# Performance work log

Hardware: AMD Instinct MI355X
Metric: run time of the kernel (lower is better)

Reference implementation:

```python
import jax, jax.numpy as jnp
import numpy as np

NUM_EXPERTS = 8
TOP_K = 2
EMBED = 1024
FFN = 2048
GATE_HID = 1024


def setup_inputs() -> dict:
    key = jax.random.key(0)
    ks = jax.random.split(key, 8)
    s_e = 1.0 / np.sqrt(EMBED)
    s_f = 1.0 / np.sqrt(FFN)
    s_g = 1.0 / np.sqrt(GATE_HID)
    return {
        "hidden_states": jax.random.normal(ks[0], (2, 2048, EMBED), dtype=jnp.float32),
        # gate: Linear(EMBED->GATE_HID) with bias, ELU, Linear(GATE_HID->NUM_EXPERTS) with bias
        "gw1": jax.random.uniform(ks[1], (EMBED, GATE_HID), jnp.float32, -s_e, s_e),
        "gb1": jax.random.uniform(ks[2], (GATE_HID,), jnp.float32, -s_e, s_e),
        "gw2": jax.random.uniform(ks[3], (GATE_HID, NUM_EXPERTS), jnp.float32, -s_g, s_g),
        "gb2": jax.random.uniform(ks[4], (NUM_EXPERTS,), jnp.float32, -s_g, s_g),
        # experts (bias=False): w1,w3: EMBED->FFN ; w2: FFN->EMBED, stacked over experts
        "w1": jax.random.uniform(ks[5], (NUM_EXPERTS, EMBED, FFN), jnp.float32, -s_e, s_e),
        "w3": jax.random.uniform(ks[6], (NUM_EXPERTS, EMBED, FFN), jnp.float32, -s_e, s_e),
        "w2": jax.random.uniform(ks[7], (NUM_EXPERTS, FFN, EMBED), jnp.float32, -s_f, s_f),
    }


def reference(hidden_states, gw1, gb1, gw2, gb2, w1, w3, w2):
    B, S, H = hidden_states.shape
    x = hidden_states.reshape(-1, H)                      # [T, H]
    T = x.shape[0]
    # gate MLP
    g = jax.nn.elu(x @ gw1 + gb1)
    router_logits = g @ gw2 + gb2                         # [T, E]
    probs = jax.nn.softmax(router_logits.astype(jnp.float32), axis=-1)
    rw, sel = jax.lax.top_k(probs, TOP_K)                 # [T, K]
    rw = rw / jnp.sum(rw, axis=-1, keepdims=True)
    rw = rw.astype(hidden_states.dtype)
    # combine weights per (token, expert); full-capacity MoE == weighted sum
    combine = jnp.zeros((T, NUM_EXPERTS), dtype=hidden_states.dtype)
    combine = combine.at[jnp.arange(T)[:, None], sel].add(rw)   # [T, E]
    # expert MLPs computed densely then combined (math identical to gather/scatter)
    h = jax.nn.relu(jnp.einsum('th,ehf->etf', x, w1)) * jnp.einsum('th,ehf->etf', x, w3)
    y = jnp.einsum('etf,efh->eth', h, w2)                 # [E, T, H]
    out = jnp.einsum('eth,te->th', y, combine)            # [T, H]
    return out.reshape(B, S, H), router_logits
```

## Files before the change

kernel.cpp:

```cpp
#include <hip/hip_runtime.h>
#include <hip/hip_bf16.h>
#include <stdint.h>

#define TOKENS 4096
#define HDIM   1024
#define FDIM   2048
#define NEXP   8
#define NSLOTS (2 * TOKENS)
#define SLOTPAD (NSLOTS + 256)
#define RISKY_CAP 256
#define FLAG_THR 6e-3f

typedef __attribute__((ext_vector_type(4))) float        f32x4v;
typedef __attribute__((ext_vector_type(4))) unsigned int u32x4v;
typedef __attribute__((ext_vector_type(8))) _Float16     f16x8v;

__device__ __forceinline__ unsigned short f2h(float f) {
  _Float16 h = (_Float16)f;
  union { _Float16 h; unsigned short u; } x; x.h = h; return x.u;
}

__device__ __forceinline__ void gload16(void* lds, const void* g) {
  __builtin_amdgcn_global_load_lds(
      reinterpret_cast<const __attribute__((address_space(1))) uint32_t*>(
          reinterpret_cast<uintptr_t>(g)),
      reinterpret_cast<__attribute__((address_space(3))) uint32_t*>(
          reinterpret_cast<uintptr_t>(lds)),
      16, 0, 0);
}

__device__ __forceinline__ void transpose_tile_v2(const float* __restrict__ ip,
                                                  unsigned short* __restrict__ op,
                                                  int R, int C, int r0, int c0) {
  __shared__ unsigned short tile[64][70];
  const int t = threadIdx.x;
  const int cp = (t & 15) * 4;
  const int rp = (t >> 4) * 2;
#pragma unroll
  for (int p = 0; p < 2; ++p) {
    const int r = rp + p * 32;
    f32x4v v0 = *(const f32x4v*)(ip + (size_t)(r0 + r) * C + c0 + cp);
    f32x4v v1 = *(const f32x4v*)(ip + (size_t)(r0 + r + 1) * C + c0 + cp);
#pragma unroll
    for (int j = 0; j < 4; ++j)
      *(uint32_t*)&tile[cp + j][r] = (uint32_t)f2h(v0[j]) | ((uint32_t)f2h(v1[j]) << 16);
  }
  __syncthreads();
  const int c = t >> 2, rc = (t & 3) * 16;
  uint32_t q[8];
#pragma unroll
  for (int j = 0; j < 8; ++j) q[j] = *(uint32_t*)&tile[c][rc + j * 2];
  unsigned short* o = op + (size_t)(c0 + c) * R + r0 + rc;
  u32x4v s0, s1;
  s0[0] = q[0]; s0[1] = q[1]; s0[2] = q[2]; s0[3] = q[3];
  s1[0] = q[4]; s1[1] = q[5]; s1[2] = q[6]; s1[3] = q[7];
  *(u32x4v*)o = s0;
  *(u32x4v*)(o + 8) = s1;
}

__global__ __launch_bounds__(256)
void k_prep0(const float* __restrict__ gw1, unsigned short* __restrict__ og1,
             int* __restrict__ rcnt) {
  if (blockIdx.x == 256) {
    if (threadIdx.x == 0) rcnt[0] = 0;
    return;
  }
  transpose_tile_v2(gw1, og1, 1024, 1024, (blockIdx.x >> 4) * 64, (blockIdx.x & 15) * 64);
}

#define NB_GATE 512
#define NB_CONV 2048
#define NB_W13  8192
#define NB_W2   4096
__global__ __launch_bounds__(256)
void k_fused(const float* __restrict__ X, unsigned short* __restrict__ Xh,
             const float* __restrict__ w1, const float* __restrict__ w3,
             unsigned short* __restrict__ o1, unsigned short* __restrict__ o3,
             const float* __restrict__ w2, unsigned short* __restrict__ o2,
             const unsigned short* __restrict__ gw1T, const float* __restrict__ gb1,
             unsigned short* __restrict__ Gh) {
  const int id = blockIdx.x;
  const int t = threadIdx.x;
  if (id < NB_GATE) {
    __shared__ unsigned short lA[128 * 64];
    __shared__ unsigned short lB[64 * 64];
    const int n0 = (id & 15) * 64, m0 = (id >> 4) * 128;
    const int lane = t & 63, wv = t >> 6;

    const unsigned short* bp[2];
#pragma unroll
    for (int i = 0; i < 2; ++i) {
      const int gi = wv * 2 + i;
      const int row = gi * 8 + (lane >> 3);
      const int cs = (lane & 7) ^ (row & 7);
      bp[i] = gw1T + (size_t)(n0 + row) * HDIM + cs * 8;
    }

    f32x4v acc[4][2];
#pragma unroll
    for (int m = 0; m < 4; ++m)
#pragma unroll
      for (int n = 0; n < 2; ++n) acc[m][n] = (f32x4v){0.f, 0.f, 0.f, 0.f};

    const int wr = (wv >> 1) * 64, wc = (wv & 1) * 32;

    for (int k0 = 0; k0 < HDIM; k0 += 64) {
#pragma unroll
      for (int p = 0; p < 4; ++p) {
        const int ga = p * 256 + t;
        const int r = ga >> 3, c = ga & 7;
        const float* s = X + (size_t)(m0 + r) * HDIM + k0 + c * 8;
        f32x4v v0 = *(const f32x4v*)s;
        f32x4v v1 = *(const f32x4v*)(s + 4);
        u32x4v pk;
        pk[0] = (uint32_t)f2h(v0[0]) | ((uint32_t)f2h(v0[1]) << 16);
        pk[1] = (uint32_t)f2h(v0[2]) | ((uint32_t)f2h(v0[3]) << 16);
        pk[2] = (uint32_t)f2h(v1[0]) | ((uint32_t)f2h(v1[1]) << 16);
        pk[3] = (uint32_t)f2h(v1[2]) | ((uint32_t)f2h(v1[3]) << 16);
        *(u32x4v*)&lA[r * 64 + ((c ^ (r & 7)) * 8)] = pk;
      }
#pragma unroll
      for (int i = 0; i < 2; ++i) gload16(lB + (wv * 2 + i) * 512, bp[i] + k0);
      __syncthreads();
#pragma unroll
      for (int kk = 0; kk < 2; ++kk) {
        const int ch = kk * 4 + (lane >> 4);
        f16x8v af[4];
#pragma unroll
        for (int m = 0; m < 4; ++m) {
          const int r = wr + m * 16 + (lane & 15);
          af[m] = *(const f16x8v*)(lA + r * 64 + (ch ^ (r & 7)) * 8);
        }
#pragma unroll
        for (int n = 0; n < 2; ++n) {
          const int r = wc + n * 16 + (lane & 15);
          f16x8v b = *(const f16x8v*)(lB + r * 64 + (ch ^ (r & 7)) * 8);
#pragma unroll
          for (int m = 0; m < 4; ++m)
            acc[m][n] = __builtin_amdgcn_mfma_f32_16x16x32_f16(af[m], b, acc[m][n], 0, 0, 0);
        }
      }
      __syncthreads();
    }
#pragma unroll
    for (int m = 0; m < 4; ++m)
#pragma unroll
      for (int n = 0; n < 2; ++n)
#pragma unroll
        for (int q = 0; q < 4; ++q) {
          const int row = m0 + wr + m * 16 + ((lane >> 4) << 2) + q;
          const int col = n0 + wc + n * 16 + (lane & 15);
          float x = acc[m][n][q] + gb1[col];
          Gh[(size_t)row * 1024 + col] = f2h(x > 0.f ? x : expm1f(x));
        }
    return;
  }
  int b = id - NB_GATE;
  if (b < NB_CONV) {
    const int i = (b * 256 + t) * 8;
    f32x4v a = *(const f32x4v*)(X + i);
    f32x4v c = *(const f32x4v*)(X + i + 4);
    u32x4v r;
    r[0] = (uint32_t)f2h(a[0]) | ((uint32_t)f2h(a[1]) << 16);
    r[1] = (uint32_t)f2h(a[2]) | ((uint32_t)f2h(a[3]) << 16);
    r[2] = (uint32_t)f2h(c[0]) | ((uint32_t)f2h(c[1]) << 16);
    r[3] = (uint32_t)f2h(c[2]) | ((uint32_t)f2h(c[3]) << 16);
    *(u32x4v*)(Xh + i) = r;
    return;
  }
  b -= NB_CONV;
  if (b < NB_W13) {
    const int bx = b & 31, by = (b >> 5) & 15, bz = b >> 9;
    const int e = bz & 7, which = bz >> 3;
    const size_t mat = (size_t)1024 * 2048;
    transpose_tile_v2((which ? w3 : w1) + (size_t)e * mat,
                      (which ? o3 : o1) + (size_t)e * mat,
                      1024, 2048, by * 64, bx * 64);
    return;
  }
  b -= NB_W13;
  {
    const int bx = b & 15, by = (b >> 4) & 31, e = b >> 9;
    const size_t mat = (size_t)2048 * 1024;
    transpose_tile_v2(w2 + (size_t)e * mat, o2 + (size_t)e * mat,
                      2048, 1024, by * 64, bx * 64);
  }
}

__global__ void k_logits(const unsigned short* __restrict__ Gh, const float* __restrict__ gw2,
                         const float* __restrict__ gb2, float* __restrict__ Lg,
                         int* __restrict__ risky, int* __restrict__ rcnt) {
  const int lane = threadIdx.x & 63, wv = threadIdx.x >> 6;
  const int tok = blockIdx.x * 4 + wv;
  const unsigned short* g = Gh + (size_t)tok * 1024 + lane * 16;
  f16x8v g0 = *(const f16x8v*)g;
  f16x8v g1 = *(const f16x8v*)(g + 8);
  float gv[16];
#pragma unroll
  for (int j = 0; j < 8; ++j) { gv[j] = (float)g0[j]; gv[8 + j] = (float)g1[j]; }
  float acc[8];
#pragma unroll
  for (int j = 0; j < 8; ++j) acc[j] = 0.f;
#pragma unroll
  for (int u = 0; u < 16; ++u) {
    const float* wrow = gw2 + (size_t)(lane * 16 + u) * 8;
    f32x4v w0 = *(const f32x4v*)wrow;
    f32x4v w1 = *(const f32x4v*)(wrow + 4);
#pragma unroll
    for (int j = 0; j < 4; ++j) {
      acc[j]     += gv[u] * w0[j];
      acc[j + 4] += gv[u] * w1[j];
    }
  }
#pragma unroll
  for (int s = 1; s < 64; s <<= 1)
#pragma unroll
    for (int j = 0; j < 8; ++j) acc[j] += __shfl_xor(acc[j], s, 64);
  if (lane == 0) {
    float l[8];
#pragma unroll
    for (int j = 0; j < 8; ++j) { l[j] = acc[j] + gb2[j]; Lg[(size_t)tok * 8 + j] = l[j]; }
    int i0 = 0; float v0 = l[0];
#pragma unroll
    for (int j = 1; j < 8; ++j) if (l[j] > v0) { v0 = l[j]; i0 = j; }
    int i1 = (i0 == 0) ? 1 : 0; float v1 = l[i1];
#pragma unroll
    for (int j = 0; j < 8; ++j) if (j != i0 && l[j] > v1) { v1 = l[j]; i1 = j; }
    float v2 = -1e30f;
#pragma unroll
    for (int j = 0; j < 8; ++j) if (j != i0 && j != i1 && l[j] > v2) v2 = l[j];
    if (v1 - v2 < FLAG_THR) {
      const int pos = atomicAdd(rcnt, 1);
      if (pos < RISKY_CAP) risky[pos] = tok;
    }
  }
}

__global__ __launch_bounds__(256)
void k_fixup_gs(const float* __restrict__ X, const float* __restrict__ gw1,
                const float* __restrict__ gb1, const int* __restrict__ risky,
                const int* __restrict__ rcnt, float* __restrict__ gsbuf) {
  __shared__ float xs[1024];
  __shared__ float red[128];
  int n = *rcnt; if (n > RISKY_CAP) n = RISKY_CAP;
  const int idx = blockIdx.y;
  if (idx >= n) return;
  const int tok = risky[idx];
  const int s0 = blockIdx.x * 128;
  const int t = threadIdx.x;
  for (int i = t; i < 1024; i += 256) xs[i] = X[(size_t)tok * 1024 + i];
  __syncthreads();
  const int h = t & 127, kh = t >> 7;
  const float* wp = gw1 + (size_t)(kh * 512) * 1024 + s0 + h;
  const float* xp = xs + kh * 512;
  float a0 = 0.f, a1 = 0.f, a2 = 0.f, a3 = 0.f;
  for (int k = 0; k < 512; k += 4) {
    a0 += xp[k]     * wp[(size_t)k * 1024];
    a1 += xp[k + 1] * wp[(size_t)(k + 1) * 1024];
    a2 += xp[k + 2] * wp[(size_t)(k + 2) * 1024];
    a3 += xp[k + 3] * wp[(size_t)(k + 3) * 1024];
  }
  const float acc = (a0 + a1) + (a2 + a3);
  if (kh == 1) red[h] = acc;
  __syncthreads();
  if (kh == 0) {
    const float v = acc + red[h] + gb1[s0 + h];
    gsbuf[(size_t)idx * 1024 + s0 + h] = v > 0.f ? v : expm1f(v);
  }
}

__global__ __launch_bounds__(256)
void k_fixup_lg(const float* __restrict__ gsbuf, const float* __restrict__ gw2,
                const float* __restrict__ gb2, const int* __restrict__ risky,
                const int* __restrict__ rcnt, float* __restrict__ Lg) {
  __shared__ float part[4][8];
  int n = *rcnt; if (n > RISKY_CAP) n = RISKY_CAP;
  const int idx = blockIdx.x;
  if (idx >= n) return;
  const int tok = risky[idx];
  const int t = threadIdx.x, lane = t & 63, wv = t >> 6;
  float lacc[8];
#pragma unroll
  for (int e = 0; e < 8; ++e) lacc[e] = 0.f;
#pragma unroll
  for (int j = 0; j < 4; ++j) {
    const int k = t * 4 + j;
    const float gv = gsbuf[(size_t)idx * 1024 + k];
    const float* w = gw2 + (size_t)k * 8;
#pragma unroll
    for (int e = 0; e < 8; ++e) lacc[e] += gv * w[e];
  }
#pragma unroll
  for (int s = 1; s < 64; s <<= 1)
#pragma unroll
    for (int e = 0; e < 8; ++e) lacc[e] += __shfl_xor(lacc[e], s, 64);
  if (lane == 0) {
#pragma unroll
    for (int e = 0; e < 8; ++e) part[wv][e] = lacc[e];
  }
  __syncthreads();
  if (t < 8) Lg[(size_t)tok * 8 + t] = part[0][t] + part[1][t] + part[2][t] + part[3][t] + gb2[t];
}

__global__ __launch_bounds__(1024)
void k_top2assign(const float* __restrict__ Lg, int* __restrict__ counts_g,
                  int* __restrict__ offs_g, int* __restrict__ slot_tok,
                  float* __restrict__ slot_w, int* __restrict__ tok2slot) {
  __shared__ int cnt[NEXP], offs[NEXP], cur[NEXP];
  const int t = threadIdx.x, lane = t & 63;
  if (t < NEXP) { cnt[t] = 0; cur[t] = 0; }
  __syncthreads();

  int te[4][2]; float tw[4][2];
#pragma unroll
  for (int p = 0; p < 4; ++p) {
    const int tok = p * 1024 + t;
    float l[8];
#pragma unroll
    for (int j = 0; j < 8; ++j) l[j] = Lg[(size_t)tok * 8 + j];
    float mx = l[0];
#pragma unroll
    for (int j = 1; j < 8; ++j) mx = fmaxf(mx, l[j]);
    float pr[8];
#pragma unroll
    for (int j = 0; j < 8; ++j) pr[j] = expf(l[j] - mx);
    int i0 = 0; float b0 = pr[0];
#pragma unroll
    for (int j = 1; j < 8; ++j) if (pr[j] > b0) { b0 = pr[j]; i0 = j; }
    int i1 = (i0 == 0) ? 1 : 0; float b1 = pr[i1];
#pragma unroll
    for (int j = 0; j < 8; ++j) if (j != i0 && pr[j] > b1) { b1 = pr[j]; i1 = j; }
    const float inv = 1.f / (b0 + b1);
    te[p][0] = i0; te[p][1] = i1;
    tw[p][0] = b0 * inv; tw[p][1] = b1 * inv;
#pragma unroll
    for (int k = 0; k < 2; ++k) {
      const int e = te[p][k];
#pragma unroll
      for (int ex = 0; ex < NEXP; ++ex) {
        const unsigned long long mask = __ballot(e == ex);
        if (mask) {
          const int leader = __ffsll((unsigned long long)mask) - 1;
          if (lane == leader) atomicAdd(&cnt[ex], (int)__popcll(mask));
        }
      }
    }
  }
  __syncthreads();
  if (t == 0) {
    int a = 0;
#pragma unroll
    for (int e = 0; e < NEXP; ++e) { offs[e] = a; a += cnt[e]; }
  }
  __syncthreads();
#pragma unroll
  for (int p = 0; p < 4; ++p) {
    const int tok = p * 1024 + t;
#pragma unroll
    for (int k = 0; k < 2; ++k) {
      const int e = te[p][k];
#pragma unroll
      for (int ex = 0; ex < NEXP; ++ex) {
        const unsigned long long mask = __ballot(e == ex);
        if (mask) {
          const int leader = __ffsll((unsigned long long)mask) - 1;
          int base = 0;
          if (lane == leader) base = atomicAdd(&cur[ex], (int)__popcll(mask));
          base = __shfl(base, leader, 64);
          if (e == ex) {
            const int s = offs[ex] + base + (int)__popcll(mask & ((1ull << lane) - 1ull));
            slot_tok[s] = tok;
            slot_w[s] = tw[p][k];
            tok2slot[2 * tok + k] = s;
          }
        }
      }
    }
  }
  if (t < NEXP) { counts_g[t] = cnt[t]; offs_g[t] = offs[t]; }
}

__global__ __launch_bounds__(256, 2)
void k_gemm1(const unsigned short* __restrict__ Xh, const unsigned short* __restrict__ w1T,
             const unsigned short* __restrict__ w3T, const int* __restrict__ slot_tok,
             const int* __restrict__ counts, const int* __restrict__ offs,
             unsigned short* __restrict__ Hout) {
  const int e = blockIdx.z;
  const int cnt = counts[e];
  const int mt = blockIdx.y;
  if (mt * 128 >= cnt) return;
  const int base = offs[e] + mt * 128;
  const int n0 = blockIdx.x * 128;

  __shared__ unsigned short lA[128 * 64];
  __shared__ unsigned short lB1[128 * 64];
  __shared__ unsigned short lB3[128 * 64];
  __shared__ int tokid[128];

  const int t = threadIdx.x;
  if (t < 128) {
    const int s = slot_tok[base + t];
    tokid[t] = ((unsigned)s < TOKENS) ? s : 0;
  }
  __syncthreads();

  const int lane = t & 63, wv = t >> 6;
  const unsigned short *arow[4], *b1row[4], *b3row[4];
#pragma unroll
  for (int i = 0; i < 4; ++i) {
    const int gi = wv * 4 + i;
    const int row = gi * 8 + (lane >> 3);
    const int cs = (lane & 7) ^ (row & 7);
    arow[i] = Xh + (size_t)tokid[row] * HDIM + cs * 8;
    const int f = n0 + row;
    b1row[i] = w1T + ((size_t)e * FDIM + f) * HDIM + cs * 8;
    b3row[i] = w3T + ((size_t)e * FDIM + f) * HDIM + cs * 8;
  }

  f32x4v acc1[4][4], acc3[4][4];
#pragma unroll
  for (int m = 0; m < 4; ++m)
#pragma unroll
    for (int n = 0; n < 4; ++n) {
      acc1[m][n] = (f32x4v){0.f, 0.f, 0.f, 0.f};
      acc3[m][n] = (f32x4v){0.f, 0.f, 0.f, 0.f};
    }
  const int wr = (wv >> 1) * 64, wc = (wv & 1) * 64;

  for (int k0 = 0; k0 < HDIM; k0 += 64) {
#pragma unroll
    for (int i = 0; i < 4; ++i) {
      gload16(lA + (wv * 4 + i) * 512, arow[i] + k0);
      gload16(lB1 + (wv * 4 + i) * 512, b1row[i] + k0);
      gload16(lB3 + (wv * 4 + i) * 512, b3row[i] + k0);
    }
    __syncthreads();
#pragma unroll
    for (int kk = 0; kk < 64; kk += 32) {
      const int ch = (kk >> 3) + (lane >> 4);
      f16x8v af[4];
#pragma unroll
      for (int m = 0; m < 4; ++m) {
        const int r = wr + m * 16 + (lane & 15);
        af[m] = *(const f16x8v*)(lA + r * 64 + (ch ^ (r & 7)) * 8);
      }
#pragma unroll
      for (int n = 0; n < 4; ++n) {
        const int r = wc + n * 16 + (lane & 15);
        const int o = r * 64 + (ch ^ (r & 7)) * 8;
        f16x8v b1 = *(const f16x8v*)(lB1 + o);
        f16x8v b3 = *(const f16x8v*)(lB3 + o);
#pragma unroll
        for (int m = 0; m < 4; ++m) {
          acc1[m][n] = __builtin_amdgcn_mfma_f32_16x16x32_f16(af[m], b1, acc1[m][n], 0, 0, 0);
          acc3[m][n] = __builtin_amdgcn_mfma_f32_16x16x32_f16(af[m], b3, acc3[m][n], 0, 0, 0);
        }
      }
    }
    __syncthreads();
  }

  const int maxr = cnt - mt * 128;
#pragma unroll
  for (int m = 0; m < 4; ++m)
#pragma unroll
    for (int q = 0; q < 4; ++q) {
      const int rl = wr + m * 16 + ((lane >> 4) << 2) + q;
      if (rl < maxr) {
        unsigned short* hrow = Hout + (size_t)(base + rl) * FDIM;
#pragma unroll
        for (int n = 0; n < 4; ++n) {
          const int col = n0 + wc + n * 16 + (lane & 15);
          const float h = fmaxf(acc1[m][n][q], 0.f) * acc3[m][n][q];
          hrow[col] = f2h(h);
        }
      }
    }
}

__global__ __launch_bounds__(256, 2)
void k_gemm2(const unsigned short* __restrict__ Hin, const unsigned short* __restrict__ w2T,
             const int* __restrict__ counts, const int* __restrict__ offs,
             unsigned short* __restrict__ Y) {
  const int e = blockIdx.z;
  const int cnt = counts[e];
  const int mt = blockIdx.y;
  if (mt * 128 >= cnt) return;
  const int base = offs[e] + mt * 128;
  const int n0 = blockIdx.x * 256;

  __shared__ unsigned short lA[128 * 64];
  __shared__ unsigned short lBa[128 * 64];
  __shared__ unsigned short lBb[128 * 64];

  const int t = threadIdx.x, lane = t & 63, wv = t >> 6;
  const unsigned short *arow[4], *browa[4], *browb[4];
#pragma unroll
  for (int i = 0; i < 4; ++i) {
    const int gi = wv * 4 + i;
    const int row = gi * 8 + (lane >> 3);
    const int cs = (lane & 7) ^ (row & 7);
    arow[i] = Hin + (size_t)(base + row) * FDIM + cs * 8;
    browa[i] = w2T + ((size_t)e * HDIM + n0 + row) * FDIM + cs * 8;
    browb[i] = w2T + ((size_t)e * HDIM + n0 + 128 + row) * FDIM + cs * 8;
  }

  f32x4v acca[4][4], accb[4][4];
#pragma unroll
  for (int m = 0; m < 4; ++m)
#pragma unroll
    for (int n = 0; n < 4; ++n) {
      acca[m][n] = (f32x4v){0.f, 0.f, 0.f, 0.f};
      accb[m][n] = (f32x4v){0.f, 0.f, 0.f, 0.f};
    }

  const int wr = (wv >> 1) * 64, wc = (wv & 1) * 64;

  for (int k0 = 0; k0 < FDIM; k0 += 64) {
#pragma unroll
    for (int i = 0; i < 4; ++i) {
      gload16(lA + (wv * 4 + i) * 512, arow[i] + k0);
      gload16(lBa + (wv * 4 + i) * 512, browa[i] + k0);
      gload16(lBb + (wv * 4 + i) * 512, browb[i] + k0);
    }
    __syncthreads();
#pragma unroll
    for (int kk = 0; kk < 64; kk += 32) {
      const int ch = (kk >> 3) + (lane >> 4);
      f16x8v af[4];
#pragma unroll
      for (int m = 0; m < 4; ++m) {
        const int r = wr + m * 16 + (lane & 15);
        af[m] = *(const f16x8v*)(lA + r * 64 + (ch ^ (r & 7)) * 8);
      }
#pragma unroll
      for (int n = 0; n < 4; ++n) {
        const int r = wc + n * 16 + (lane & 15);
        const int o = r * 64 + (ch ^ (r & 7)) * 8;
        f16x8v ba = *(const f16x8v*)(lBa + o);
        f16x8v bb = *(const f16x8v*)(lBb + o);
#pragma unroll
        for (int m = 0; m < 4; ++m) {
          acca[m][n] = __builtin_amdgcn_mfma_f32_16x16x32_f16(af[m], ba, acca[m][n], 0, 0, 0);
          accb[m][n] = __builtin_amdgcn_mfma_f32_16x16x32_f16(af[m], bb, accb[m][n], 0, 0, 0);
        }
      }
    }
    __syncthreads();
  }

  const int maxr = cnt - mt * 128;
#pragma unroll
  for (int m = 0; m < 4; ++m)
#pragma unroll
    for (int q = 0; q < 4; ++q) {
      const int rl = wr + m * 16 + ((lane >> 4) << 2) + q;
      if (rl < maxr) {
        unsigned short* yrow = Y + (size_t)(base + rl) * HDIM;
#pragma unroll
        for (int n = 0; n < 4; ++n) {
          const int col = n0 + wc + n * 16 + (lane & 15);
          yrow[col] = f2h(acca[m][n][q]);
          yrow[col + 128] = f2h(accb[m][n][q]);
        }
      }
    }
}

__global__ __launch_bounds__(256)
void k_combine(const unsigned short* __restrict__ Y, const int* __restrict__ tok2slot,
               const float* __restrict__ slot_w, float* __restrict__ out) {
  const int tok = blockIdx.x;
  const int s0 = tok2slot[2 * tok], s1 = tok2slot[2 * tok + 1];
  const float w0 = slot_w[s0], w1 = slot_w[s1];
  const int i = threadIdx.x * 4;
  const _Float16* y0 = (const _Float16*)(Y + (size_t)s0 * HDIM + i);
  const _Float16* y1 = (const _Float16*)(Y + (size_t)s1 * HDIM + i);
  f32x4v r;
#pragma unroll
  for (int j = 0; j < 4; ++j) r[j] = w0 * (float)y0[j] + w1 * (float)y1[j];
  *(f32x4v*)(out + (size_t)tok * HDIM + i) = r;
}

extern "C" void kernel_launch(void* const* d_in, const int* in_sizes, int n_in,
                              void* d_out, int out_size, void* d_ws, size_t ws_size,
                              hipStream_t stream) {
  const float* X   = (const float*)d_in[0];
  const float* gw1 = (const float*)d_in[1];
  const float* gb1 = (const float*)d_in[2];
  const float* gw2 = (const float*)d_in[3];
  const float* gb2 = (const float*)d_in[4];
  const float* w1  = (const float*)d_in[5];
  const float* w3  = (const float*)d_in[6];
  const float* w2  = (const float*)d_in[7];

  float* out = (float*)d_out;
  float* Lg  = out + (size_t)TOKENS * HDIM;

  char* ws = (char*)d_ws;
  size_t off = 0;
  auto alloc = [&](size_t b) { void* p = ws + off; off = (off + b + 255) & ~(size_t)255; return p; };

  unsigned short* Xh    = (unsigned short*)alloc((size_t)TOKENS * HDIM * 2);
  unsigned short* gw1T  = (unsigned short*)alloc((size_t)HDIM * 1024 * 2);
  unsigned short* w1T   = (unsigned short*)alloc((size_t)NEXP * FDIM * HDIM * 2);
  unsigned short* w3T   = (unsigned short*)alloc((size_t)NEXP * FDIM * HDIM * 2);
  unsigned short* w2T   = (unsigned short*)alloc((size_t)NEXP * HDIM * FDIM * 2);
  unsigned short* Gh    = (unsigned short*)alloc((size_t)TOKENS * 1024 * 2);
  unsigned short* Hf    = (unsigned short*)alloc((size_t)SLOTPAD * FDIM * 2);
  unsigned short* Yb    = (unsigned short*)alloc((size_t)SLOTPAD * HDIM * 2);
  float*          gsbuf = (float*)alloc((size_t)RISKY_CAP * 1024 * 4);
  int*   tok2slot = (int*)alloc((size_t)TOKENS * 2 * 4);
  int*   counts   = (int*)alloc(64);
  int*   offs     = (int*)alloc(64);
  int*   slot_tok = (int*)alloc((size_t)SLOTPAD * 4);
  float* slot_w   = (float*)alloc((size_t)SLOTPAD * 4);
  int*   risky    = (int*)alloc((size_t)RISKY_CAP * 4);
  int*   rcnt     = (int*)alloc(64);

  k_prep0<<<dim3(257), 256, 0, stream>>>(gw1, gw1T, rcnt);
  k_fused<<<dim3(NB_GATE + NB_CONV + NB_W13 + NB_W2), 256, 0, stream>>>(
      X, Xh, w1, w3, w1T, w3T, w2, w2T, gw1T, gb1, Gh);
  k_logits<<<dim3(TOKENS / 4), 256, 0, stream>>>(Gh, gw2, gb2, Lg, risky, rcnt);
  k_fixup_gs<<<dim3(8, RISKY_CAP), 256, 0, stream>>>(X, gw1, gb1, risky, rcnt, gsbuf);
  k_fixup_lg<<<dim3(RISKY_CAP), 256, 0, stream>>>(gsbuf, gw2, gb2, risky, rcnt, Lg);
  k_top2assign<<<dim3(1), 1024, 0, stream>>>(Lg, counts, offs, slot_tok, slot_w, tok2slot);
  k_gemm1<<<dim3(FDIM / 128, TOKENS / 128, NEXP), 256, 0, stream>>>(Xh, w1T, w3T, slot_tok, counts, offs, Hf);
  k_gemm2<<<dim3(HDIM / 256, TOKENS / 128, NEXP), 256, 0, stream>>>(Hf, w2T, counts, offs, Yb);
  k_combine<<<dim3(TOKENS), 256, 0, stream>>>(Yb, tok2slot, slot_w, out);
}
```

Measured before the change: 318.9 us.

## Split-K gemm2 into two halves and fold logit fixup into top2 assign

The down-projection GEMM is split along the FFN dimension into two K halves. Each half writes its own fp16 partial Y buffer, and the combine kernel sums the two partials. This doubles the number of blocks to fill more CUs, at the cost of twice the Y write/read traffic and an extra fp16 rounding step. The separate risky-token logit fixup kernel is also merged into the single-block top-2 assignment kernel, removing one launch but doing that work inside a single workgroup.

Measured after the change: 405.9 us. 1.27x slower.

```diff
diff --git a/kernel.cpp b/kernel.cpp
--- a/kernel.cpp
+++ b/kernel.cpp
@@ -269,55 +269,64 @@
   }
 }
 
-__global__ __launch_bounds__(256)
-void k_fixup_lg(const float* __restrict__ gsbuf, const float* __restrict__ gw2,
-                const float* __restrict__ gb2, const int* __restrict__ risky,
-                const int* __restrict__ rcnt, float* __restrict__ Lg) {
-  __shared__ float part[4][8];
+__global__ __launch_bounds__(1024)
+void k_top2assign(const float* __restrict__ Lg, const float* __restrict__ gsbuf,
+                  const float* __restrict__ gw2, const float* __restrict__ gb2,
+                  const int* __restrict__ risky, const int* __restrict__ rcnt,
+                  int* __restrict__ counts_g, int* __restrict__ offs_g,
+                  int* __restrict__ slot_tok, float* __restrict__ slot_w,
+                  int* __restrict__ tok2slot, float* __restrict__ Lg_out) {
+  __shared__ int cnt[NEXP], offs[NEXP], cur[NEXP];
+  __shared__ short fixslot[TOKENS];
+  __shared__ float lgfix[RISKY_CAP][8];
+  const int t = threadIdx.x, lane = t & 63, wv = t >> 6;
+  for (int i = t; i < TOKENS; i += 1024) fixslot[i] = -1;
+  if (t < NEXP) { cnt[t] = 0; cur[t] = 0; }
   int n = *rcnt; if (n > RISKY_CAP) n = RISKY_CAP;
-  const int idx = blockIdx.x;
-  if (idx >= n) return;
-  const int tok = risky[idx];
-  const int t = threadIdx.x, lane = t & 63, wv = t >> 6;
-  float lacc[8];
-#pragma unroll
-  for (int e = 0; e < 8; ++e) lacc[e] = 0.f;
-#pragma unroll
-  for (int j = 0; j < 4; ++j) {
-    const int k = t * 4 + j;
-    const float gv = gsbuf[(size_t)idx * 1024 + k];
-    const float* w = gw2 + (size_t)k * 8;
-#pragma unroll
-    for (int e = 0; e < 8; ++e) lacc[e] += gv * w[e];
-  }
-#pragma unroll
-  for (int s = 1; s < 64; s <<= 1)
-#pragma unroll
-    for (int e = 0; e < 8; ++e) lacc[e] += __shfl_xor(lacc[e], s, 64);
-  if (lane == 0) {
-#pragma unroll
-    for (int e = 0; e < 8; ++e) part[wv][e] = lacc[e];
-  }
-  __syncthreads();
-  if (t < 8) Lg[(size_t)tok * 8 + t] = part[0][t] + part[1][t] + part[2][t] + part[3][t] + gb2[t];
-}
-
-__global__ __launch_bounds__(1024)
-void k_top2assign(const float* __restrict__ Lg, int* __restrict__ counts_g,
-                  int* __restrict__ offs_g, int* __restrict__ slot_tok,
-                  float* __restrict__ slot_w, int* __restrict__ tok2slot) {
-  __shared__ int cnt[NEXP], offs[NEXP], cur[NEXP];
-  const int t = threadIdx.x, lane = t & 63;
-  if (t < NEXP) { cnt[t] = 0; cur[t] = 0; }
+  __syncthreads();
+
+  for (int idx = wv; idx < n; idx += 16) {
+    const int tok = risky[idx];
+    float lacc[8];
+#pragma unroll
+    for (int e = 0; e < 8; ++e) lacc[e] = 0.f;
+#pragma unroll
+    for (int j = 0; j < 16; ++j) {
+      const int k = lane * 16 + j;
+      const float gv = gsbuf[(size_t)idx * 1024 + k];
+      const float* w = gw2 + (size_t)k * 8;
+#pragma unroll
+      for (int e = 0; e < 8; ++e) lacc[e] += gv * w[e];
+    }
+#pragma unroll
+    for (int s = 1; s < 64; s <<= 1)
+#pragma unroll
+      for (int e = 0; e < 8; ++e) lacc[e] += __shfl_xor(lacc[e], s, 64);
+    if (lane == 0) {
+#pragma unroll
+      for (int e = 0; e < 8; ++e) {
+        const float v = lacc[e] + gb2[e];
+        lgfix[idx][e] = v;
+        Lg_out[(size_t)tok * 8 + e] = v;
+      }
+      fixslot[tok] = (short)idx;
+    }
+  }
   __syncthreads();
 
   int te[4][2]; float tw[4][2];
 #pragma unroll
   for (int p = 0; p < 4; ++p) {
     const int tok = p * 1024 + t;
+    const int fs = fixslot[tok];
     float l[8];
-#pragma unroll
-    for (int j = 0; j < 8; ++j) l[j] = Lg[(size_t)tok * 8 + j];
+    if (fs >= 0) {
+#pragma unroll
+      for (int j = 0; j < 8; ++j) l[j] = lgfix[fs][j];
+    } else {
+#pragma unroll
+      for (int j = 0; j < 8; ++j) l[j] = Lg[(size_t)tok * 8 + j];
+    }
     float mx = l[0];
 #pragma unroll
     for (int j = 1; j < 8; ++j) mx = fmaxf(mx, l[j]);
@@ -482,12 +491,14 @@
 void k_gemm2(const unsigned short* __restrict__ Hin, const unsigned short* __restrict__ w2T,
              const int* __restrict__ counts, const int* __restrict__ offs,
              unsigned short* __restrict__ Y) {
-  const int e = blockIdx.z;
+  const int z = blockIdx.z;
+  const int e = z >> 1, kh = z & 1;
   const int cnt = counts[e];
   const int mt = blockIdx.y;
   if (mt * 128 >= cnt) return;
   const int base = offs[e] + mt * 128;
   const int n0 = blockIdx.x * 256;
+  const int kbeg = kh * (FDIM / 2);
 
   __shared__ unsigned short lA[128 * 64];
   __shared__ unsigned short lBa[128 * 64];
@@ -500,9 +511,9 @@
     const int gi = wv * 4 + i;
     const int row = gi * 8 + (lane >> 3);
     const int cs = (lane & 7) ^ (row & 7);
-    arow[i] = Hin + (size_t)(base + row) * FDIM + cs * 8;
-    browa[i] = w2T + ((size_t)e * HDIM + n0 + row) * FDIM + cs * 8;
-    browb[i] = w2T + ((size_t)e * HDIM + n0 + 128 + row) * FDIM + cs * 8;
+    arow[i] = Hin + (size_t)(base + row) * FDIM + kbeg + cs * 8;
+    browa[i] = w2T + ((size_t)e * HDIM + n0 + row) * FDIM + kbeg + cs * 8;
+    browb[i] = w2T + ((size_t)e * HDIM + n0 + 128 + row) * FDIM + kbeg + cs * 8;
   }
 
   f32x4v acca[4][4], accb[4][4];
@@ -516,7 +527,7 @@
 
   const int wr = (wv >> 1) * 64, wc = (wv & 1) * 64;
 
-  for (int k0 = 0; k0 < FDIM; k0 += 64) {
+  for (int k0 = 0; k0 < FDIM / 2; k0 += 64) {
 #pragma unroll
     for (int i = 0; i < 4; ++i) {
       gload16(lA + (wv * 4 + i) * 512, arow[i] + k0);
@@ -549,6 +560,7 @@
     __syncthreads();
   }
 
+  unsigned short* Yp = Y + (size_t)kh * SLOTPAD * HDIM;
   const int maxr = cnt - mt * 128;
 #pragma unroll
   for (int m = 0; m < 4; ++m)
@@ -556,7 +568,7 @@
     for (int q = 0; q < 4; ++q) {
       const int rl = wr + m * 16 + ((lane >> 4) << 2) + q;
       if (rl < maxr) {
-        unsigned short* yrow = Y + (size_t)(base + rl) * HDIM;
+        unsigned short* yrow = Yp + (size_t)(base + rl) * HDIM;
 #pragma unroll
         for (int n = 0; n < 4; ++n) {
           const int col = n0 + wc + n * 16 + (lane & 15);
@@ -574,11 +586,15 @@
   const int s0 = tok2slot[2 * tok], s1 = tok2slot[2 * tok + 1];
   const float w0 = slot_w[s0], w1 = slot_w[s1];
   const int i = threadIdx.x * 4;
-  const _Float16* y0 = (const _Float16*)(Y + (size_t)s0 * HDIM + i);
-  const _Float16* y1 = (const _Float16*)(Y + (size_t)s1 * HDIM + i);
+  const size_t P = (size_t)SLOTPAD * HDIM;
+  const _Float16* y00 = (const _Float16*)(Y + (size_t)s0 * HDIM + i);
+  const _Float16* y01 = (const _Float16*)(Y + P + (size_t)s0 * HDIM + i);
+  const _Float16* y10 = (const _Float16*)(Y + (size_t)s1 * HDIM + i);
+  const _Float16* y11 = (const _Float16*)(Y + P + (size_t)s1 * HDIM + i);
   f32x4v r;
 #pragma unroll
-  for (int j = 0; j < 4; ++j) r[j] = w0 * (float)y0[j] + w1 * (float)y1[j];
+  for (int j = 0; j < 4; ++j)
+    r[j] = w0 * ((float)y00[j] + (float)y01[j]) + w1 * ((float)y10[j] + (float)y11[j]);
   *(f32x4v*)(out + (size_t)tok * HDIM + i) = r;
 }
 
@@ -608,7 +624,7 @@
   unsigned short* w2T   = (unsigned short*)alloc((size_t)NEXP * HDIM * FDIM * 2);
   unsigned short* Gh    = (unsigned short*)alloc((size_t)TOKENS * 1024 * 2);
   unsigned short* Hf    = (unsigned short*)alloc((size_t)SLOTPAD * FDIM * 2);
-  unsigned short* Yb    = (unsigned short*)alloc((size_t)SLOTPAD * HDIM * 2);
+  unsigned short* Yb    = (unsigned short*)alloc((size_t)2 * SLOTPAD * HDIM * 2);
   float*          gsbuf = (float*)alloc((size_t)RISKY_CAP * 1024 * 4);
   int*   tok2slot = (int*)alloc((size_t)TOKENS * 2 * 4);
   int*   counts   = (int*)alloc(64);
@@ -623,9 +639,9 @@
       X, Xh, w1, w3, w1T, w3T, w2, w2T, gw1T, gb1, Gh);
   k_logits<<<dim3(TOKENS / 4), 256, 0, stream>>>(Gh, gw2, gb2, Lg, risky, rcnt);
   k_fixup_gs<<<dim3(8, RISKY_CAP), 256, 0, stream>>>(X, gw1, gb1, risky, rcnt, gsbuf);
-  k_fixup_lg<<<dim3(RISKY_CAP), 256, 0, stream>>>(gsbuf, gw2, gb2, risky, rcnt, Lg);
-  k_top2assign<<<dim3(1), 1024, 0, stream>>>(Lg, counts, offs, slot_tok, slot_w, tok2slot);
+  k_top2assign<<<dim3(1), 1024, 0, stream>>>(Lg, gsbuf, gw2, gb2, risky, rcnt,
+                                             counts, offs, slot_tok, slot_w, tok2slot, Lg);
   k_gemm1<<<dim3(FDIM / 128, TOKENS / 128, NEXP), 256, 0, stream>>>(Xh, w1T, w3T, slot_tok, counts, offs, Hf);
-  k_gemm2<<<dim3(HDIM / 256, TOKENS / 128, NEXP), 256, 0, stream>>>(Hf, w2T, counts, offs, Yb);
+  k_gemm2<<<dim3(HDIM / 256, TOKENS / 128, NEXP * 2), 256, 0, stream>>>(Hf, w2T, counts, offs, Yb);
   k_combine<<<dim3(TOKENS), 256, 0, stream>>>(Yb, tok2slot, slot_w, out);
 }
```
